# Optimization experiments

Measured on AMD Instinct MI355X. Metric: run time of the kernel, lower is better.

Reference implementation:

```python
import jax, jax.numpy as jnp
import numpy as np

NUM_CLASSES = 80
BATCH_PER_IMG = 512
FG_CAP = 128  # int(512 * 0.25)
IOU_THRESH = 0.5
STRIDE = 16.0
OUT = 7
RATIO = 2


def _pairwise_iou(gt, pr):
    # gt: [M,4], pr: [N,4] in (x1,y1,x2,y2) -> [M,N]
    area_g = (gt[:, 2] - gt[:, 0]) * (gt[:, 3] - gt[:, 1])
    area_p = (pr[:, 2] - pr[:, 0]) * (pr[:, 3] - pr[:, 1])
    lt = jnp.maximum(gt[:, None, :2], pr[None, :, :2])
    rb = jnp.minimum(gt[:, None, 2:], pr[None, :, 2:])
    wh = jnp.clip(rb - lt, 0.0)
    inter = wh[..., 0] * wh[..., 1]
    union = area_g[:, None] + area_p[None, :] - inter
    return jnp.where(inter > 0, inter / union, 0.0)


def _match_and_sample(iou, gt_cls, rand):
    # iou: [M,N]; Matcher(thresholds=[0.5], labels=[0,1], no low-quality)
    matched_vals = iou.max(axis=0)
    matched_idxs = iou.argmax(axis=0)
    matched = matched_vals >= IOU_THRESH
    cls = jnp.where(matched, gt_cls[matched_idxs], NUM_CLASSES)
    fg = cls != NUM_CLASSES
    bg = ~fg

    def _rank(mask):
        # rank of each masked element under random permutation (rand in [0,1))
        key = jnp.where(mask, rand, 2.0)
        return jnp.argsort(jnp.argsort(key))

    num_fg = jnp.minimum(fg.sum(), FG_CAP)
    sel_fg = fg & (_rank(fg) < num_fg)
    num_bg = jnp.minimum(BATCH_PER_IMG - num_fg, bg.sum())
    sel_bg = bg & (_rank(bg) < num_bg)
    score = sel_fg * 2.0 + sel_bg * 1.0
    _, sampled = jax.lax.top_k(score, BATCH_PER_IMG)
    return sampled, cls[sampled], matched_idxs[sampled]


def _roi_align(feat, rois, batch_idx):
    # feat: [B,C,H,W], rois: [R,4] image coords, aligned=True ROIAlignV2
    B, C, H, W = feat.shape
    f = feat.transpose(0, 2, 3, 1)  # [B,H,W,C]
    b = rois / STRIDE - 0.5
    x1, y1, x2, y2 = b[:, 0], b[:, 1], b[:, 2], b[:, 3]
    g = (jnp.arange(OUT * RATIO, dtype=feat.dtype) + 0.5) / RATIO  # [14] in bin units
    xs = x1[:, None] + g[None, :] * ((x2 - x1) / OUT)[:, None]  # [R,14]
    ys = y1[:, None] + g[None, :] * ((y2 - y1) / OUT)[:, None]
    xs = jnp.clip(xs, 0.0, W - 1)
    ys = jnp.clip(ys, 0.0, H - 1)
    x0 = jnp.floor(xs).astype(jnp.int32)
    y0 = jnp.floor(ys).astype(jnp.int32)
    x1i = jnp.minimum(x0 + 1, W - 1)
    y1i = jnp.minimum(y0 + 1, H - 1)
    lx = xs - x0.astype(xs.dtype)
    ly = ys - y0.astype(ys.dtype)
    bb = batch_idx[:, None, None]
    v00 = f[bb, y0[:, :, None], x0[:, None, :]]  # [R,14,14,C]
    v01 = f[bb, y0[:, :, None], x1i[:, None, :]]
    v10 = f[bb, y1i[:, :, None], x0[:, None, :]]
    v11 = f[bb, y1i[:, :, None], x1i[:, None, :]]
    wy1 = ly[:, :, None, None]
    wy0 = 1.0 - wy1
    wx1 = lx[:, None, :, None]
    wx0 = 1.0 - wx1
    val = v00 * wy0 * wx0 + v01 * wy0 * wx1 + v10 * wy1 * wx0 + v11 * wy1 * wx1
    R = rois.shape[0]
    pooled = val.reshape(R, OUT, RATIO, OUT, RATIO, C).mean(axis=(2, 4))  # [R,7,7,C]
    return pooled.transpose(0, 3, 1, 2).reshape(R, -1)  # channel-major flatten, matches torch


def setup_inputs() -> dict:
    key = jax.random.key(0)
    ks = jax.random.split(key, 14)
    B, N, M, C, H, W = 2, 2000, 64, 256, 64, 64
    IMG = 1024.0

    def mk_boxes(k, b, n):
        pts = jax.random.uniform(k, (b, n, 2, 2), jnp.float32) * (IMG - 16.0)
        lo = pts.min(axis=2)
        hi = pts.max(axis=2) + 8.0
        return jnp.concatenate([lo, hi], axis=-1)

    D = C * OUT * OUT  # 12544
    FC = 1024
    return {
        "features": jax.random.normal(ks[0], (B, C, H, W), jnp.float32),
        "proposal_boxes": mk_boxes(ks[1], B, N),
        "gt_boxes": mk_boxes(ks[2], B, M),
        "gt_classes": jax.random.randint(ks[3], (B, M), 0, NUM_CLASSES),
        "rand_scores": jax.random.uniform(ks[4], (B, N + M), jnp.float32),
        "fc1_w": jax.random.normal(ks[5], (D, FC), jnp.float32) * 0.02,
        "fc1_b": jnp.zeros((FC,), jnp.float32),
        "fc2_w": jax.random.normal(ks[6], (FC, FC), jnp.float32) * 0.02,
        "fc2_b": jnp.zeros((FC,), jnp.float32),
        "cls_w": jax.random.normal(ks[7], (FC, NUM_CLASSES + 1), jnp.float32) * 0.02,
        "cls_b": jnp.zeros((NUM_CLASSES + 1,), jnp.float32),
        "box_w": jax.random.normal(ks[8], (FC, NUM_CLASSES * 4), jnp.float32) * 0.02,
        "box_b": jnp.zeros((NUM_CLASSES * 4,), jnp.float32),
    }


def reference(features, proposal_boxes, gt_boxes, gt_classes, rand_scores,
              fc1_w, fc1_b, fc2_w, fc2_b, cls_w, cls_b, box_w, box_b):
    # proposal_append_gt: concat GT boxes onto proposals
    all_boxes = jnp.concatenate([proposal_boxes, gt_boxes], axis=1)  # [B,N+M,4]
    iou = jax.vmap(_pairwise_iou)(gt_boxes, all_boxes)  # [B,M,N+M]
    sampled, cls, _ = jax.vmap(_match_and_sample)(iou, gt_classes, rand_scores)
    rois = jnp.take_along_axis(all_boxes, sampled[..., None], axis=1).reshape(-1, 4)
    B = features.shape[0]
    bidx = jnp.repeat(jnp.arange(B), BATCH_PER_IMG)
    x = _roi_align(features, rois, bidx)  # [R, 12544]
    x = jax.nn.relu(x @ fc1_w + fc1_b)
    x = jax.nn.relu(x @ fc2_w + fc2_b)
    out = jnp.concatenate([x @ cls_w + cls_b, x @ box_w + box_b], axis=-1)  # [R, 401]
    return out
```

## Files before the change

### kernel.cpp

```cpp
#include <hip/hip_runtime.h>
#include <cstdint>
#include <cstddef>

constexpr int B_   = 2;
constexpr int N_   = 2000;
constexpr int M_   = 64;
constexpr int NB_  = N_ + M_;
constexpr int C_   = 256;
constexpr int H_   = 64;
constexpr int W_   = 64;
constexpr int RPI  = 512;
constexpr int RTOT = B_ * RPI;
constexpr int FG_CAP_ = 128;
constexpr int D_   = C_ * 49;
constexpr int FC_  = 1024;
constexpr int OUTC = 401;
constexpr int KT1  = D_ / 32;
constexpr int KT2  = FC_ / 32;
constexpr float IOU_T = 0.5f;

typedef _Float16 f16;
typedef f16   f16x2 __attribute__((ext_vector_type(2)));
typedef f16   f16x8 __attribute__((ext_vector_type(8)));
typedef float f32x4 __attribute__((ext_vector_type(4)));

__device__ __forceinline__ void tile_load16(const void* g, void* l) {
  __builtin_amdgcn_global_load_lds(
      (const __attribute__((address_space(1))) unsigned int*)g,
      (__attribute__((address_space(3))) unsigned int*)l, 16, 0, 0);
}

__global__ __launch_bounds__(256) void k_transpose(const float* __restrict__ in,
                                                   f16* __restrict__ out) {
  __shared__ float tile[64][33];
  int b = blockIdx.z, hw0 = blockIdx.x * 32, c0 = blockIdx.y * 64;
  int t = threadIdx.x;
  int tx = t & 31, cr0 = t >> 5;
#pragma unroll
  for (int i = 0; i < 8; ++i) {
    int cr = cr0 + i * 8;
    tile[cr][tx] = in[((size_t)b * C_ + c0 + cr) * (H_ * W_) + hw0 + tx];
  }
  __syncthreads();
  int c2 = (t & 31) * 2, hr0 = t >> 5;
#pragma unroll
  for (int p = 0; p < 4; ++p) {
    int hr = hr0 + p * 8;
    f16x2 v;
    v[0] = (f16)tile[c2][hr];
    v[1] = (f16)tile[c2 + 1][hr];
    *(f16x2*)(out + ((size_t)b * (H_ * W_) + hw0 + hr) * C_ + c0 + c2) = v;
  }
}

__global__ __launch_bounds__(1024) void k_iou(const float* __restrict__ prop,
                                              const float* __restrict__ gt,
                                              unsigned char* __restrict__ fg,
                                              int* __restrict__ cnt) {
  __shared__ float s_gt[M_ * 4];
  __shared__ float s_area[M_];
  __shared__ int s_cnt;
  int b = blockIdx.x, t = threadIdx.x;
  if (t == 0) s_cnt = 0;
  if (t < M_ * 4) s_gt[t] = gt[(size_t)b * M_ * 4 + t];
  __syncthreads();
  if (t < M_) {
    float x1 = s_gt[t*4], y1 = s_gt[t*4+1], x2 = s_gt[t*4+2], y2 = s_gt[t*4+3];
    s_area[t] = (x2 - x1) * (y2 - y1);
  }
  __syncthreads();
  int local = 0;
  for (int j = t; j < NB_; j += 1024) {
    float bx1, by1, bx2, by2;
    if (j < N_) {
      const float* p = prop + ((size_t)b * N_ + j) * 4;
      bx1 = p[0]; by1 = p[1]; bx2 = p[2]; by2 = p[3];
    } else {
      const float* p = s_gt + (j - N_) * 4;
      bx1 = p[0]; by1 = p[1]; bx2 = p[2]; by2 = p[3];
    }
    float area_p = (bx2 - bx1) * (by2 - by1);
    float best = 0.f;
    for (int g = 0; g < M_; ++g) {
      float lx = fmaxf(s_gt[g*4], bx1),   lyv = fmaxf(s_gt[g*4+1], by1);
      float rx = fminf(s_gt[g*4+2], bx2), ry  = fminf(s_gt[g*4+3], by2);
      float w = fmaxf(rx - lx, 0.f), h = fmaxf(ry - lyv, 0.f);
      float inter = w * h;
      float iou = inter > 0.f ? inter / (s_area[g] + area_p - inter) : 0.f;
      best = fmaxf(best, iou);
    }
    int f = (best >= IOU_T) ? 1 : 0;
    fg[(size_t)b * NB_ + j] = (unsigned char)f;
    local += f;
  }
  atomicAdd(&s_cnt, local);
  __syncthreads();
  if (t == 0) cnt[b] = s_cnt;
}

__global__ __launch_bounds__(256) void k_rank(const float* __restrict__ rnd,
                                              const unsigned char* __restrict__ fg,
                                              const int* __restrict__ cnt,
                                              unsigned char* __restrict__ sel) {
  __shared__ unsigned long long s_key[NB_];
  int b = blockIdx.y, t = threadIdx.x;
  for (int j = t; j < NB_; j += 256) {
    float r = rnd[(size_t)b * NB_ + j];
    int f = (int)fg[(size_t)b * NB_ + j];
    float ck = r + 2.0f * (float)f;
    unsigned int ib = __float_as_uint(ck);
    s_key[j] = ((unsigned long long)ib << 11) | (unsigned int)j;
  }
  __syncthreads();
  int j = blockIdx.x * 256 + t;
  int jj = (j < NB_) ? j : 0;
  unsigned long long uj = s_key[jj];
  int rank_all = 0;
  const uint4* kp = (const uint4*)s_key;
#pragma unroll 4
  for (int k2 = 0; k2 < NB_ / 2; ++k2) {
    uint4 v = kp[k2];
    unsigned long long k0 = ((unsigned long long)v.y << 32) | v.x;
    unsigned long long k1 = ((unsigned long long)v.w << 32) | v.z;
    rank_all += (k0 < uj) ? 1 : 0;
    rank_all += (k1 < uj) ? 1 : 0;
  }
  if (j >= NB_) return;
  int fgcnt  = cnt[b];
  int num_fg = min(fgcnt, FG_CAP_);
  int num_bg = min(RPI - num_fg, NB_ - fgcnt);
  int myfg   = (uj >> 11) >= 0x40000000ull ? 1 : 0;
  int rank   = rank_all - (myfg ? (NB_ - fgcnt) : 0);
  int lim    = myfg ? num_fg : num_bg;
  sel[(size_t)b * NB_ + j] =
      (rank < lim) ? (unsigned char)(myfg ? 2 : 1) : (unsigned char)0;
}

__global__ __launch_bounds__(64) void k_place(const float* __restrict__ prop,
                                              const float* __restrict__ gt,
                                              const int* __restrict__ cnt,
                                              const unsigned char* __restrict__ sel,
                                              float* __restrict__ rois) {
  int b = blockIdx.x, L = threadIdx.x;
  int fgcnt  = cnt[b];
  int num_fg = min(fgcnt, FG_CAP_);
  int num_bg = min(RPI - num_fg, NB_ - fgcnt);
  int S = num_fg + num_bg;
  int t2 = 0, t1 = 0, t0 = 0;
  unsigned long long lt = (L == 0) ? 0ull : ((~0ull) >> (64 - L));
  for (int c = 0; c < (NB_ + 63) / 64; ++c) {
    int j = c * 64 + L;
    int s = (j < NB_) ? (int)sel[(size_t)b * NB_ + j] : -1;
    unsigned long long m2 = __ballot(s == 2);
    unsigned long long m1 = __ballot(s == 1);
    unsigned long long m0 = __ballot(s == 0);
    int pos = -1;
    if (s == 2) {
      pos = t2 + __popcll(m2 & lt);
    } else if (s == 1) {
      pos = num_fg + t1 + __popcll(m1 & lt);
    } else if (s == 0) {
      int p0 = t0 + __popcll(m0 & lt);
      if (S + p0 < RPI) pos = S + p0;
    }
    if (pos >= 0) {
      const float* p = (j < N_) ? (prop + ((size_t)b * N_ + j) * 4)
                                : (gt + ((size_t)b * M_ + (j - N_)) * 4);
      float* o = rois + ((size_t)b * RPI + pos) * 4;
      o[0] = p[0]; o[1] = p[1]; o[2] = p[2]; o[3] = p[3];
    }
    t2 += __popcll(m2); t1 += __popcll(m1); t0 += __popcll(m0);
  }
}

__global__ __launch_bounds__(256) void k_roialign(const f16* __restrict__ fT,
                                                  const float* __restrict__ rois,
                                                  f16* __restrict__ Ahi) {
  __shared__ float sv[8][260];
  __shared__ int   s_off[32][4];
  __shared__ float s_w[32][4];
  int mt = blockIdx.x, bin = blockIdx.y;
  int tid = threadIdx.x;
  int by = bin / 7, bx = bin % 7;
  for (int pass = 0; pass < 2; ++pass) {
    if (tid < 32) {
      int rr = tid >> 2, s = tid & 3;
      int r = mt * 16 + pass * 8 + rr;
      const float* rp = rois + (size_t)r * 4;
      float x1 = rp[0] * 0.0625f - 0.5f;
      float y1 = rp[1] * 0.0625f - 0.5f;
      float x2 = rp[2] * 0.0625f - 0.5f;
      float y2 = rp[3] * 0.0625f - 0.5f;
      float stx = (x2 - x1) * (1.0f / 7.0f);
      float sty = (y2 - y1) * (1.0f / 7.0f);
      int oy = s >> 1, ox = s & 1;
      float xs = x1 + ((float)(2 * bx + ox) + 0.5f) * 0.5f * stx;
      float ys = y1 + ((float)(2 * by + oy) + 0.5f) * 0.5f * sty;
      xs = fminf(fmaxf(xs, 0.f), (float)(W_ - 1));
      ys = fminf(fmaxf(ys, 0.f), (float)(H_ - 1));
      int x0 = (int)floorf(xs), y0 = (int)floorf(ys);
      int x1i = min(x0 + 1, W_ - 1), y1i = min(y0 + 1, H_ - 1);
      float lx = xs - (float)x0, ly = ys - (float)y0;
      int base = (r >> 9) * (H_ * W_ * C_);
      s_off[tid][0] = base + (y0  * W_ + x0 ) * C_;
      s_off[tid][1] = base + (y0  * W_ + x1i) * C_;
      s_off[tid][2] = base + (y1i * W_ + x0 ) * C_;
      s_off[tid][3] = base + (y1i * W_ + x1i) * C_;
      s_w[tid][0] = (1.f - ly) * (1.f - lx);
      s_w[tid][1] = (1.f - ly) * lx;
      s_w[tid][2] = ly * (1.f - lx);
      s_w[tid][3] = ly * lx;
    }
    __syncthreads();
    {
      int rr = tid >> 5;
      int c0 = (tid & 31) * 8;
      float acc[8] = {};
#pragma unroll
      for (int s = 0; s < 4; ++s) {
        int e = rr * 4 + s;
#pragma unroll
        for (int q = 0; q < 4; ++q) {
          int off = s_off[e][q];
          float w = s_w[e][q];
          f16x8 v = *(const f16x8*)(fT + off + c0);
#pragma unroll
          for (int k = 0; k < 8; ++k) acc[k] += w * (float)v[k];
        }
      }
#pragma unroll
      for (int k = 0; k < 8; ++k) sv[rr][c0 + k] = acc[k] * 0.25f;
    }
    __syncthreads();
    int c = tid;
    int kt = c >> 5;
    int l5 = c & 31;
    int quad = l5 >> 3;
    int r8 = l5 & 7;
    int lane = quad * 16 + pass * 8 + r8;
    int cbase = kt * 32 + quad * 8;
    f16x8 hv;
#pragma unroll
    for (int jj = 0; jj < 8; ++jj) hv[jj] = (f16)sv[r8][cbase + jj];
    size_t off = ((size_t)(mt * KT1 + bin * 8 + kt) * 64 + lane) * 8;
    *(f16x8*)(Ahi + off) = hv;
    __syncthreads();
  }
}

__global__ __launch_bounds__(256) void k_convw(const float* __restrict__ src,
                                               const float* __restrict__ src2,
                                               f16* __restrict__ dst,
                                               int KTtot, int mode) {
  __shared__ float tile[32][65];
  int kt = blockIdx.x, ng = blockIdx.y;
  int t = threadIdx.x;
  int n0 = ng * 64;
  int col = t & 63;
#pragma unroll
  for (int p = 0; p < 8; ++p) {
    int r = p * 4 + (t >> 6);
    int k = kt * 32 + r;
    float v;
    if (mode == 0) {
      v = src[(size_t)k * 1024 + n0 + col];
    } else if (mode == 1) {
      int row = (k & 255) * 49 + (k >> 8);
      v = src[(size_t)row * 1024 + n0 + col];
    } else {
      int n = n0 + col;
      v = (n < 81) ? src[(size_t)k * 81 + n]
                   : ((n < 401) ? src2[(size_t)k * 320 + (n - 81)] : 0.f);
    }
    tile[r][col] = v;
  }
  __syncthreads();
  int sub = t >> 6, lane = t & 63;
  int nt = ng * 4 + sub;
  int nl = lane & 15, kg = lane >> 4;
  f16x8 h;
#pragma unroll
  for (int e = 0; e < 8; ++e)
    h[e] = (f16)tile[kg * 8 + e][sub * 16 + nl];
  *(f16x8*)(dst + ((size_t)(nt * KTtot + kt) * 64 + lane) * 8) = h;
}

__global__ __launch_bounds__(256, 2) void k_gemm_mfma(
    const f16* __restrict__ Ahi, const f16* __restrict__ Bw,
    float* __restrict__ P, int N, int KTtot, int ktPerSplit) {
  __shared__ f16 sA[16 * 512];
  __shared__ f16 sB[16 * 512];
  int tid = threadIdx.x;
  int lane = tid & 63, w = tid >> 6;
  int wm = w >> 1, wn = w & 1;
  int bn = blockIdx.x, bm = blockIdx.y, z = blockIdx.z;
  int kt0 = z * ktPerSplit, ktEnd = kt0 + ktPerSplit;

  f32x4 acc[4][4];
#pragma unroll
  for (int i = 0; i < 4; ++i)
#pragma unroll
    for (int j = 0; j < 4; ++j) {
      f32x4 zv = {0.f, 0.f, 0.f, 0.f};
      acc[i][j] = zv;
    }

  int kt = kt0;
  for (; kt + 1 < ktEnd; kt += 2) {
#pragma unroll
    for (int tt = 0; tt < 8; ++tt) {
      int t = 8 * w + tt;
      int k2 = t >> 4;
      int tl = t & 15;
      const f16* g;
      f16* l;
      if (tl < 8) { g = Ahi + ((size_t)(bm*8 + tl)     * KTtot + kt + k2) * 512; l = sA + (k2*8 + tl) * 512; }
      else        { g = Bw  + ((size_t)(bn*8 + tl - 8) * KTtot + kt + k2) * 512; l = sB + (k2*8 + tl - 8) * 512; }
      tile_load16(g + lane * 8, l);
    }
    __syncthreads();
#pragma unroll
    for (int k2 = 0; k2 < 2; ++k2) {
      f16x8 ah[4], bw[4];
#pragma unroll
      for (int i = 0; i < 4; ++i) {
        ah[i] = *(const f16x8*)(sA + (k2*8 + wm*4 + i) * 512 + lane * 8);
        bw[i] = *(const f16x8*)(sB + (k2*8 + wn*4 + i) * 512 + lane * 8);
      }
#pragma unroll
      for (int i = 0; i < 4; ++i)
#pragma unroll
        for (int j = 0; j < 4; ++j)
          acc[i][j] = __builtin_amdgcn_mfma_f32_16x16x32_f16(ah[i], bw[j], acc[i][j], 0, 0, 0);
    }
    __syncthreads();
  }
  if (kt < ktEnd) {
#pragma unroll
    for (int tt = 0; tt < 4; ++tt) {
      int t = 4 * w + tt;
      const f16* g;
      f16* l;
      if (t < 8) { g = Ahi + ((size_t)(bm*8 + t)     * KTtot + kt) * 512; l = sA + t * 512; }
      else       { g = Bw  + ((size_t)(bn*8 + t - 8) * KTtot + kt) * 512; l = sB + (t - 8) * 512; }
      tile_load16(g + lane * 8, l);
    }
    __syncthreads();
    f16x8 ah[4], bw[4];
#pragma unroll
    for (int i = 0; i < 4; ++i) {
      ah[i] = *(const f16x8*)(sA + (wm*4 + i) * 512 + lane * 8);
      bw[i] = *(const f16x8*)(sB + (wn*4 + i) * 512 + lane * 8);
    }
#pragma unroll
    for (int i = 0; i < 4; ++i)
#pragma unroll
      for (int j = 0; j < 4; ++j)
        acc[i][j] = __builtin_amdgcn_mfma_f32_16x16x32_f16(ah[i], bw[j], acc[i][j], 0, 0, 0);
    __syncthreads();
  }

  int quad = lane >> 4, cl = lane & 15;
  float* Pz = P + (size_t)z * 1024 * (size_t)N;
#pragma unroll
  for (int i = 0; i < 4; ++i) {
    int row = bm * 128 + wm * 64 + i * 16 + quad * 4;
#pragma unroll
    for (int j = 0; j < 4; ++j) {
      int col = bn * 128 + wn * 64 + j * 16 + cl;
#pragma unroll
      for (int r = 0; r < 4; ++r)
        Pz[(size_t)(row + r) * N + col] = acc[i][j][r];
    }
  }
}

__global__ __launch_bounds__(256) void k_combine(const float* __restrict__ P,
                                                 const float* __restrict__ bias,
                                                 f16* __restrict__ Ahi,
                                                 int nsplit) {
  int q = blockIdx.x * 256 + threadIdx.x;
  int lane = q & 63, tile = q >> 6;
  int mt = tile >> 5, kt = tile & 31;
  int m  = mt * 16 + (lane & 15);
  int n0 = kt * 32 + (lane >> 4) * 8;
  float v[8];
#pragma unroll
  for (int jj = 0; jj < 8; ++jj) v[jj] = bias[n0 + jj];
  for (int s = 0; s < nsplit; ++s) {
    const float* p = P + (size_t)s * 1048576 + (size_t)m * 1024 + n0;
#pragma unroll
    for (int jj = 0; jj < 8; ++jj) v[jj] += p[jj];
  }
  f16x8 hv;
#pragma unroll
  for (int jj = 0; jj < 8; ++jj) hv[jj] = (f16)fmaxf(v[jj], 0.f);
  *(f16x8*)(Ahi + (size_t)q * 8) = hv;
}

__global__ __launch_bounds__(256) void k_out(const float* __restrict__ P,
                                             const float* __restrict__ cls_b,
                                             const float* __restrict__ box_b,
                                             float* __restrict__ out, int nsplit) {
  int idx = blockIdx.x * 256 + threadIdx.x;
  if (idx >= RTOT * OUTC) return;
  int m = idx / OUTC, n = idx - m * OUTC;
  float v = (n < 81) ? cls_b[n] : box_b[n - 81];
  for (int s = 0; s < nsplit; ++s)
    v += P[(size_t)s * (1024 * 512) + (size_t)m * 512 + n];
  out[idx] = v;
}

extern "C" void kernel_launch(void* const* d_in, const int* in_sizes, int n_in,
                              void* d_out, int out_size, void* d_ws, size_t ws_size,
                              hipStream_t stream) {
  const float* features = (const float*)d_in[0];
  const float* prop     = (const float*)d_in[1];
  const float* gt       = (const float*)d_in[2];
  const float* rnd      = (const float*)d_in[4];
  const float* fc1_w    = (const float*)d_in[5];
  const float* fc1_b    = (const float*)d_in[6];
  const float* fc2_w    = (const float*)d_in[7];
  const float* fc2_b    = (const float*)d_in[8];
  const float* cls_w    = (const float*)d_in[9];
  const float* cls_b    = (const float*)d_in[10];
  const float* box_w    = (const float*)d_in[11];
  const float* box_b    = (const float*)d_in[12];
  float* out = (float*)d_out;

  char* base = (char*)d_ws;
  f16*   fT   = (f16*)(base + 0);
  float* rois = (float*)(base + 8388608);
  char*  p2   = base + 8404992;
  f16* A1hi = (f16*)(base + 8404992);
  f16* W1   = (f16*)(base + 34095104);
  float* P1 = (float*)(base + 59785216);
  int s1 = (ws_size >= (size_t)59785216 + 8ull * 4194304) ? 8 : 4;
  f16* A2hi = (f16*)(p2 + 0);
  f16* W2   = (f16*)(p2 + 2097152);
  f16* A3hi = (f16*)(p2 + 4194304);
  f16* W3   = (f16*)(p2 + 6291456);
  float* P2 = (float*)(p2 + 7340032);
  float* P3 = (float*)(p2 + 24117248);
  unsigned char* g_fg  = (unsigned char*)(base + 59785216);
  unsigned char* g_sel = (unsigned char*)(base + 59785216 + 4160);
  int*           g_cnt = (int*)(base + 59785216 + 8320);

  k_transpose<<<dim3(128, 4, B_), dim3(256), 0, stream>>>(features, fT);
  k_iou<<<dim3(B_), dim3(1024), 0, stream>>>(prop, gt, g_fg, g_cnt);
  k_rank<<<dim3((NB_ + 255) / 256, B_), dim3(256), 0, stream>>>(rnd, g_fg, g_cnt, g_sel);
  k_place<<<dim3(B_), dim3(64), 0, stream>>>(prop, gt, g_cnt, g_sel, rois);
  k_roialign<<<dim3(64, 49), dim3(256), 0, stream>>>(fT, rois, A1hi);
  k_convw<<<dim3(KT1, 16), dim3(256), 0, stream>>>(fc1_w, nullptr, W1, KT1, 1);
  k_gemm_mfma<<<dim3(8, 8, s1), dim3(256), 0, stream>>>(A1hi, W1, P1,
                                                        1024, KT1, KT1 / s1);
  k_combine<<<dim3(512), dim3(256), 0, stream>>>(P1, fc1_b, A2hi, s1);
  k_convw<<<dim3(KT2, 16), dim3(256), 0, stream>>>(fc2_w, nullptr, W2, KT2, 0);
  k_gemm_mfma<<<dim3(8, 8, 4), dim3(256), 0, stream>>>(A2hi, W2, P2,
                                                       1024, KT2, KT2 / 4);
  k_combine<<<dim3(512), dim3(256), 0, stream>>>(P2, fc2_b, A3hi, 4);
  k_convw<<<dim3(KT2, 8), dim3(256), 0, stream>>>(cls_w, box_w, W3, KT2, 2);
  k_gemm_mfma<<<dim3(4, 8, 4), dim3(256), 0, stream>>>(A3hi, W3, P3,
                                                       512, KT2, KT2 / 4);
  k_out<<<dim3((RTOT * OUTC + 255) / 256), dim3(256), 0, stream>>>(
      P3, cls_b, box_b, out, 4);
}
```

Baseline: 320.0 us.

## Merge small kernels into combined launches and raise fc1 split-K to 14

```diff
diff --git a/kernel.cpp b/kernel.cpp
--- a/kernel.cpp
+++ b/kernel.cpp
@@ -30,72 +30,74 @@
       (__attribute__((address_space(3))) unsigned int*)l, 16, 0, 0);
 }
 
-__global__ __launch_bounds__(256) void k_transpose(const float* __restrict__ in,
-                                                   f16* __restrict__ out) {
-  __shared__ float tile[64][33];
-  int b = blockIdx.z, hw0 = blockIdx.x * 32, c0 = blockIdx.y * 64;
+__global__ __launch_bounds__(256) void k_tiou(
+    const float* __restrict__ feat, const float* __restrict__ prop,
+    const float* __restrict__ gtb, f16* __restrict__ fT,
+    unsigned char* __restrict__ fg, int* __restrict__ cnt) {
+  __shared__ __align__(16) char smem[8448];
+  int bid = blockIdx.x;
   int t = threadIdx.x;
-  int tx = t & 31, cr0 = t >> 5;
-#pragma unroll
-  for (int i = 0; i < 8; ++i) {
-    int cr = cr0 + i * 8;
-    tile[cr][tx] = in[((size_t)b * C_ + c0 + cr) * (H_ * W_) + hw0 + tx];
-  }
-  __syncthreads();
-  int c2 = (t & 31) * 2, hr0 = t >> 5;
-#pragma unroll
-  for (int p = 0; p < 4; ++p) {
-    int hr = hr0 + p * 8;
-    f16x2 v;
-    v[0] = (f16)tile[c2][hr];
-    v[1] = (f16)tile[c2 + 1][hr];
-    *(f16x2*)(out + ((size_t)b * (H_ * W_) + hw0 + hr) * C_ + c0 + c2) = v;
-  }
-}
-
-__global__ __launch_bounds__(1024) void k_iou(const float* __restrict__ prop,
-                                              const float* __restrict__ gt,
-                                              unsigned char* __restrict__ fg,
-                                              int* __restrict__ cnt) {
-  __shared__ float s_gt[M_ * 4];
-  __shared__ float s_area[M_];
-  __shared__ int s_cnt;
-  int b = blockIdx.x, t = threadIdx.x;
-  if (t == 0) s_cnt = 0;
-  if (t < M_ * 4) s_gt[t] = gt[(size_t)b * M_ * 4 + t];
-  __syncthreads();
-  if (t < M_) {
-    float x1 = s_gt[t*4], y1 = s_gt[t*4+1], x2 = s_gt[t*4+2], y2 = s_gt[t*4+3];
-    s_area[t] = (x2 - x1) * (y2 - y1);
-  }
-  __syncthreads();
-  int local = 0;
-  for (int j = t; j < NB_; j += 1024) {
-    float bx1, by1, bx2, by2;
-    if (j < N_) {
-      const float* p = prop + ((size_t)b * N_ + j) * 4;
-      bx1 = p[0]; by1 = p[1]; bx2 = p[2]; by2 = p[3];
-    } else {
-      const float* p = s_gt + (j - N_) * 4;
-      bx1 = p[0]; by1 = p[1]; bx2 = p[2]; by2 = p[3];
-    }
-    float area_p = (bx2 - bx1) * (by2 - by1);
-    float best = 0.f;
-    for (int g = 0; g < M_; ++g) {
-      float lx = fmaxf(s_gt[g*4], bx1),   lyv = fmaxf(s_gt[g*4+1], by1);
-      float rx = fminf(s_gt[g*4+2], bx2), ry  = fminf(s_gt[g*4+3], by2);
-      float w = fmaxf(rx - lx, 0.f), h = fmaxf(ry - lyv, 0.f);
-      float inter = w * h;
-      float iou = inter > 0.f ? inter / (s_area[g] + area_p - inter) : 0.f;
-      best = fmaxf(best, iou);
-    }
-    int f = (best >= IOU_T) ? 1 : 0;
-    fg[(size_t)b * NB_ + j] = (unsigned char)f;
-    local += f;
-  }
-  atomicAdd(&s_cnt, local);
-  __syncthreads();
-  if (t == 0) cnt[b] = s_cnt;
+  if (bid < 1024) {
+    float (*tile)[33] = (float(*)[33])smem;
+    int b = bid >> 9, rem = bid & 511;
+    int hw0 = (rem & 127) * 32, c0 = ((rem >> 7) & 3) * 64;
+    int tx = t & 31, cr0 = t >> 5;
+#pragma unroll
+    for (int i = 0; i < 8; ++i) {
+      int cr = cr0 + i * 8;
+      tile[cr][tx] = feat[((size_t)b * C_ + c0 + cr) * (H_ * W_) + hw0 + tx];
+    }
+    __syncthreads();
+    int c2 = (t & 31) * 2, hr0 = t >> 5;
+#pragma unroll
+    for (int p = 0; p < 4; ++p) {
+      int hr = hr0 + p * 8;
+      f16x2 v;
+      v[0] = (f16)tile[c2][hr];
+      v[1] = (f16)tile[c2 + 1][hr];
+      *(f16x2*)(fT + ((size_t)b * (H_ * W_) + hw0 + hr) * C_ + c0 + c2) = v;
+    }
+  } else {
+    float* s_gt   = (float*)smem;
+    float* s_area = (float*)(smem + 1024);
+    int*   s_cnt  = (int*)(smem + 1280);
+    int b = bid - 1024;
+    if (t == 0) *s_cnt = 0;
+    s_gt[t] = gtb[(size_t)b * M_ * 4 + t];
+    __syncthreads();
+    if (t < M_) {
+      float x1 = s_gt[t*4], y1 = s_gt[t*4+1], x2 = s_gt[t*4+2], y2 = s_gt[t*4+3];
+      s_area[t] = (x2 - x1) * (y2 - y1);
+    }
+    __syncthreads();
+    int local = 0;
+    for (int j = t; j < NB_; j += 256) {
+      float bx1, by1, bx2, by2;
+      if (j < N_) {
+        const float* p = prop + ((size_t)b * N_ + j) * 4;
+        bx1 = p[0]; by1 = p[1]; bx2 = p[2]; by2 = p[3];
+      } else {
+        const float* p = s_gt + (j - N_) * 4;
+        bx1 = p[0]; by1 = p[1]; bx2 = p[2]; by2 = p[3];
+      }
+      float area_p = (bx2 - bx1) * (by2 - by1);
+      float best = 0.f;
+      for (int g = 0; g < M_; ++g) {
+        float lx = fmaxf(s_gt[g*4], bx1),   lyv = fmaxf(s_gt[g*4+1], by1);
+        float rx = fminf(s_gt[g*4+2], bx2), ry  = fminf(s_gt[g*4+3], by2);
+        float w = fmaxf(rx - lx, 0.f), h = fmaxf(ry - lyv, 0.f);
+        float inter = w * h;
+        float iou = inter > 0.f ? inter / (s_area[g] + area_p - inter) : 0.f;
+        best = fmaxf(best, iou);
+      }
+      int f = (best >= IOU_T) ? 1 : 0;
+      fg[(size_t)b * NB_ + j] = (unsigned char)f;
+      local += f;
+    }
+    atomicAdd(s_cnt, local);
+    __syncthreads();
+    if (t == 0) cnt[b] = *s_cnt;
+  }
 }
 
 __global__ __launch_bounds__(256) void k_rank(const float* __restrict__ rnd,
@@ -248,32 +250,22 @@
   }
 }
 
-__global__ __launch_bounds__(256) void k_convw(const float* __restrict__ src,
-                                               const float* __restrict__ src2,
-                                               f16* __restrict__ dst,
-                                               int KTtot, int mode) {
+__global__ __launch_bounds__(256) void k_convw1(const float* __restrict__ src,
+                                                f16* __restrict__ dst) {
   __shared__ float tile[32][65];
   int kt = blockIdx.x, ng = blockIdx.y;
   int t = threadIdx.x;
   int n0 = ng * 64;
   int col = t & 63;
+  float vv[8];
 #pragma unroll
   for (int p = 0; p < 8; ++p) {
-    int r = p * 4 + (t >> 6);
-    int k = kt * 32 + r;
-    float v;
-    if (mode == 0) {
-      v = src[(size_t)k * 1024 + n0 + col];
-    } else if (mode == 1) {
-      int row = (k & 255) * 49 + (k >> 8);
-      v = src[(size_t)row * 1024 + n0 + col];
-    } else {
-      int n = n0 + col;
-      v = (n < 81) ? src[(size_t)k * 81 + n]
-                   : ((n < 401) ? src2[(size_t)k * 320 + (n - 81)] : 0.f);
-    }
-    tile[r][col] = v;
-  }
+    int k = kt * 32 + p * 4 + (t >> 6);
+    int row = (k & 255) * 49 + (k >> 8);
+    vv[p] = src[(size_t)row * 1024 + n0 + col];
+  }
+#pragma unroll
+  for (int p = 0; p < 8; ++p) tile[p * 4 + (t >> 6)][col] = vv[p];
   __syncthreads();
   int sub = t >> 6, lane = t & 63;
   int nt = ng * 4 + sub;
@@ -282,7 +274,7 @@
 #pragma unroll
   for (int e = 0; e < 8; ++e)
     h[e] = (f16)tile[kg * 8 + e][sub * 16 + nl];
-  *(f16x8*)(dst + ((size_t)(nt * KTtot + kt) * 64 + lane) * 8) = h;
+  *(f16x8*)(dst + ((size_t)(nt * KT1 + kt) * 64 + lane) * 8) = h;
 }
 
 __global__ __launch_bounds__(256, 2) void k_gemm_mfma(
@@ -305,8 +297,7 @@
       acc[i][j] = zv;
     }
 
-  int kt = kt0;
-  for (; kt + 1 < ktEnd; kt += 2) {
+  for (int kt = kt0; kt + 1 < ktEnd; kt += 2) {
 #pragma unroll
     for (int tt = 0; tt < 8; ++tt) {
       int t = 8 * w + tt;
@@ -335,30 +326,6 @@
     }
     __syncthreads();
   }
-  if (kt < ktEnd) {
-#pragma unroll
-    for (int tt = 0; tt < 4; ++tt) {
-      int t = 4 * w + tt;
-      const f16* g;
-      f16* l;
-      if (t < 8) { g = Ahi + ((size_t)(bm*8 + t)     * KTtot + kt) * 512; l = sA + t * 512; }
-      else       { g = Bw  + ((size_t)(bn*8 + t - 8) * KTtot + kt) * 512; l = sB + (t - 8) * 512; }
-      tile_load16(g + lane * 8, l);
-    }
-    __syncthreads();
-    f16x8 ah[4], bw[4];
-#pragma unroll
-    for (int i = 0; i < 4; ++i) {
-      ah[i] = *(const f16x8*)(sA + (wm*4 + i) * 512 + lane * 8);
-      bw[i] = *(const f16x8*)(sB + (wn*4 + i) * 512 + lane * 8);
-    }
-#pragma unroll
-    for (int i = 0; i < 4; ++i)
-#pragma unroll
-      for (int j = 0; j < 4; ++j)
-        acc[i][j] = __builtin_amdgcn_mfma_f32_16x16x32_f16(ah[i], bw[j], acc[i][j], 0, 0, 0);
-    __syncthreads();
-  }
 
   int quad = lane >> 4, cl = lane & 15;
   float* Pz = P + (size_t)z * 1024 * (size_t)N;
@@ -375,27 +342,61 @@
   }
 }
 
-__global__ __launch_bounds__(256) void k_combine(const float* __restrict__ P,
-                                                 const float* __restrict__ bias,
-                                                 f16* __restrict__ Ahi,
-                                                 int nsplit) {
-  int q = blockIdx.x * 256 + threadIdx.x;
-  int lane = q & 63, tile = q >> 6;
-  int mt = tile >> 5, kt = tile & 31;
-  int m  = mt * 16 + (lane & 15);
-  int n0 = kt * 32 + (lane >> 4) * 8;
-  float v[8];
-#pragma unroll
-  for (int jj = 0; jj < 8; ++jj) v[jj] = bias[n0 + jj];
-  for (int s = 0; s < nsplit; ++s) {
-    const float* p = P + (size_t)s * 1048576 + (size_t)m * 1024 + n0;
-#pragma unroll
-    for (int jj = 0; jj < 8; ++jj) v[jj] += p[jj];
-  }
-  f16x8 hv;
-#pragma unroll
-  for (int jj = 0; jj < 8; ++jj) hv[jj] = (f16)fmaxf(v[jj], 0.f);
-  *(f16x8*)(Ahi + (size_t)q * 8) = hv;
+__global__ __launch_bounds__(256) void k_mid(
+    const float* __restrict__ P, const float* __restrict__ bias,
+    f16* __restrict__ Adst, int nsplit,
+    const float* __restrict__ wsrc, const float* __restrict__ wsrc2,
+    f16* __restrict__ Wdst, int wmode) {
+  __shared__ float tile[32][65];
+  int bid = blockIdx.x;
+  int t = threadIdx.x;
+  if (bid < 512) {
+    int q = bid * 256 + t;
+    int lane = q & 63, tl = q >> 6;
+    int mt = tl >> 5, kt = tl & 31;
+    int m  = mt * 16 + (lane & 15);
+    int n0 = kt * 32 + (lane >> 4) * 8;
+    float v[8];
+#pragma unroll
+    for (int jj = 0; jj < 8; ++jj) v[jj] = bias[n0 + jj];
+    for (int s = 0; s < nsplit; ++s) {
+      const float* p = P + (size_t)s * 1048576 + (size_t)m * 1024 + n0;
+#pragma unroll
+      for (int jj = 0; jj < 8; ++jj) v[jj] += p[jj];
+    }
+    f16x8 hv;
+#pragma unroll
+    for (int jj = 0; jj < 8; ++jj) hv[jj] = (f16)fmaxf(v[jj], 0.f);
+    *(f16x8*)(Adst + (size_t)q * 8) = hv;
+  } else {
+    int cb = bid - 512;
+    int kt = cb & 31, ng = cb >> 5;
+    int n0 = ng * 64;
+    int col = t & 63;
+    float vv[8];
+#pragma unroll
+    for (int p = 0; p < 8; ++p) {
+      int k = kt * 32 + p * 4 + (t >> 6);
+      if (wmode == 0) {
+        vv[p] = wsrc[(size_t)k * 1024 + n0 + col];
+      } else {
+        int n = n0 + col;
+        vv[p] = (n < 81) ? wsrc[(size_t)k * 81 + n]
+                         : ((n < 401) ? wsrc2[(size_t)k * 320 + (n - 81)] : 0.f);
+      }
+    }
+#pragma unroll
+    for (int p = 0; p < 8; ++p) tile[p * 4 + (t >> 6)][col] = vv[p];
+    __syncthreads();
+    int sub = t >> 6, lane = t & 63;
+    int nt = ng * 4 + sub;
+    int nl = lane & 15, kg = lane >> 4;
+    f16x8 h;
+#pragma unroll
+    for (int e = 0; e < 8; ++e)
+      h[e] = (f16)tile[kg * 8 + e][sub * 16 + nl];
+    *(f16x8*)(Wdst + ((size_t)(nt * 32 + kt) * 64 + lane) * 8) = h;
+  }
 }
 
 __global__ __launch_bounds__(256) void k_out(const float* __restrict__ P,
@@ -435,7 +436,7 @@
   f16* A1hi = (f16*)(base + 8404992);
   f16* W1   = (f16*)(base + 34095104);
   float* P1 = (float*)(base + 59785216);
-  int s1 = (ws_size >= (size_t)59785216 + 8ull * 4194304) ? 8 : 4;
+  int s1 = (ws_size >= (size_t)59785216 + 14ull * 4194304) ? 14 : 8;
   f16* A2hi = (f16*)(p2 + 0);
   f16* W2   = (f16*)(p2 + 2097152);
   f16* A3hi = (f16*)(p2 + 4194304);
@@ -446,20 +447,20 @@
   unsigned char* g_sel = (unsigned char*)(base + 59785216 + 4160);
   int*           g_cnt = (int*)(base + 59785216 + 8320);
 
-  k_transpose<<<dim3(128, 4, B_), dim3(256), 0, stream>>>(features, fT);
-  k_iou<<<dim3(B_), dim3(1024), 0, stream>>>(prop, gt, g_fg, g_cnt);
+  k_tiou<<<dim3(1026), dim3(256), 0, stream>>>(features, prop, gt, fT,
+                                               g_fg, g_cnt);
   k_rank<<<dim3((NB_ + 255) / 256, B_), dim3(256), 0, stream>>>(rnd, g_fg, g_cnt, g_sel);
   k_place<<<dim3(B_), dim3(64), 0, stream>>>(prop, gt, g_cnt, g_sel, rois);
   k_roialign<<<dim3(64, 49), dim3(256), 0, stream>>>(fT, rois, A1hi);
-  k_convw<<<dim3(KT1, 16), dim3(256), 0, stream>>>(fc1_w, nullptr, W1, KT1, 1);
+  k_convw1<<<dim3(KT1, 16), dim3(256), 0, stream>>>(fc1_w, W1);
   k_gemm_mfma<<<dim3(8, 8, s1), dim3(256), 0, stream>>>(A1hi, W1, P1,
                                                         1024, KT1, KT1 / s1);
-  k_combine<<<dim3(512), dim3(256), 0, stream>>>(P1, fc1_b, A2hi, s1);
-  k_convw<<<dim3(KT2, 16), dim3(256), 0, stream>>>(fc2_w, nullptr, W2, KT2, 0);
+  k_mid<<<dim3(1024), dim3(256), 0, stream>>>(P1, fc1_b, A2hi, s1,
+                                              fc2_w, nullptr, W2, 0);
   k_gemm_mfma<<<dim3(8, 8, 4), dim3(256), 0, stream>>>(A2hi, W2, P2,
                                                        1024, KT2, KT2 / 4);
-  k_combine<<<dim3(512), dim3(256), 0, stream>>>(P2, fc2_b, A3hi, 4);
-  k_convw<<<dim3(KT2, 8), dim3(256), 0, stream>>>(cls_w, box_w, W3, KT2, 2);
+  k_mid<<<dim3(768), dim3(256), 0, stream>>>(P2, fc2_b, A3hi, 4,
+                                             cls_w, box_w, W3, 2);
   k_gemm_mfma<<<dim3(4, 8, 4), dim3(256), 0, stream>>>(A3hi, W3, P3,
                                                        512, KT2, KT2 / 4);
   k_out<<<dim3((RTOT * OUTC + 255) / 256), dim3(256), 0, stream>>>(
```

Measured after the change: 361.0 us. 1.13x slower.
